# Kernel optimization log

Hardware: AMD Instinct MI355X
Metric: run time of the kernel (lower is better)

## Reference

```python
import jax, jax.numpy as jnp
import numpy as np

B, S_Q, S_KV = 4, 2048, 2048
D_MODEL, HEADS, D_QK, D_V = 1024, 16, 64, 64


def setup_inputs() -> dict:
    key = jax.random.key(0)
    ks = jax.random.split(key, 12)
    s = lambda fan_in: 1.0 / np.sqrt(fan_in)
    return {
        "x": jax.random.normal(ks[0], (B, S_Q, D_MODEL), jnp.float32),
        "encoder_output": jax.random.normal(ks[1], (B, S_KV, D_MODEL), jnp.float32),
        # per-head Linear weights stacked over heads: [H, D_MODEL, d_head]
        "Wq": jax.random.uniform(ks[2], (HEADS, D_MODEL, D_QK), jnp.float32, -s(D_MODEL), s(D_MODEL)),
        "bq": jax.random.uniform(ks[3], (HEADS, D_QK), jnp.float32, -s(D_MODEL), s(D_MODEL)),
        "Wk": jax.random.uniform(ks[4], (HEADS, D_MODEL, D_QK), jnp.float32, -s(D_MODEL), s(D_MODEL)),
        "bk": jax.random.uniform(ks[5], (HEADS, D_QK), jnp.float32, -s(D_MODEL), s(D_MODEL)),
        "Wv": jax.random.uniform(ks[6], (HEADS, D_MODEL, D_V), jnp.float32, -s(D_MODEL), s(D_MODEL)),
        "bv": jax.random.uniform(ks[7], (HEADS, D_V), jnp.float32, -s(D_MODEL), s(D_MODEL)),
        # output Linear: [H*D_V, D_MODEL]
        "Wo": jax.random.uniform(ks[8], (HEADS * D_V, D_MODEL), jnp.float32, -s(HEADS * D_V), s(HEADS * D_V)),
        "bo": jax.random.uniform(ks[9], (D_MODEL,), jnp.float32, -s(HEADS * D_V), s(HEADS * D_V)),
    }


def reference(x, encoder_output, Wq, bq, Wk, bk, Wv, bv, Wo, bo):
    # Batched equivalent of the per-head Python loop: project all heads at once.
    q = jnp.einsum("bqd,hde->bhqe", x, Wq) + bq[None, :, None, :]              # [B,H,Sq,dk]
    k = jnp.einsum("bsd,hde->bhse", encoder_output, Wk) + bk[None, :, None, :]  # [B,H,Skv,dk]
    v = jnp.einsum("bsd,hde->bhse", encoder_output, Wv) + bv[None, :, None, :]  # [B,H,Skv,dv]
    scale = 1.0 / jnp.sqrt(jnp.asarray(D_QK, x.dtype))
    scores = jnp.einsum("bhqe,bhse->bhqs", q, k) * scale                        # [B,H,Sq,Skv]
    attn = jax.nn.softmax(scores, axis=-1)
    heads = jnp.einsum("bhqs,bhse->bhqe", attn, v)                              # [B,H,Sq,dv]
    # concat heads on last dim (head order matches the torch list concat)
    multihead = heads.transpose(0, 2, 1, 3).reshape(x.shape[0], x.shape[1], HEADS * D_V)
    return multihead @ Wo + bo
```

## Files before the change

### kernel.cpp

```cpp
#include <hip/hip_runtime.h>
#include <hip/hip_bf16.h>
#include <stdint.h>

typedef unsigned short u16;
typedef __bf16 bf16x8 __attribute__((ext_vector_type(8)));
typedef float f32x4 __attribute__((ext_vector_type(4)));
typedef float f32x16 __attribute__((ext_vector_type(16)));
typedef unsigned short us8 __attribute__((ext_vector_type(8)));

__device__ __forceinline__ u16 f2bf(float f) {
  union { float f; uint32_t u; } v; v.f = f;
  uint32_t u = v.u;
  return (u16)((u + 0x7FFFu + ((u >> 16) & 1u)) >> 16);
}

__device__ __forceinline__ uint32_t cvtpk(float a, float b) {
  uint32_t r;
  asm("v_cvt_pk_bf16_f32 %0, %1, %2" : "=v"(r) : "v"(a), "v"(b));
  return r;
}

__device__ __forceinline__ void gload_lds16(const void* g, void* l) {
  __builtin_amdgcn_global_load_lds(
      (const __attribute__((address_space(1))) void*)(uintptr_t)g,
      (__attribute__((address_space(3))) void*)(uint32_t)(uintptr_t)l,
      16, 0, 0);
}

__device__ __forceinline__ float vsum16(f32x16 v) {
  float a = (v[0] + v[1]) + (v[2] + v[3]);
  float b = (v[4] + v[5]) + (v[6] + v[7]);
  float c = (v[8] + v[9]) + (v[10] + v[11]);
  float d = (v[12] + v[13]) + (v[14] + v[15]);
  return (a + b) + (c + d);
}

#define CROW(r, g) (((r) & 3) + 8 * ((r) >> 2) + 4 * (g))

__global__ __launch_bounds__(256) void cvt_all_k(
    const float* __restrict__ x, const float* __restrict__ enc,
    const float* __restrict__ Wq, const float* __restrict__ Wk,
    const float* __restrict__ Wv, const float* __restrict__ Wo,
    u16* __restrict__ xb, u16* __restrict__ eb,
    u16* __restrict__ wqb, u16* __restrict__ wkb,
    u16* __restrict__ wvb, u16* __restrict__ wob) {
  __shared__ float t[64][65];
  const int blk = blockIdx.x;
  const int tid = threadIdx.x;

  if (blk < 8192) {
    const float* in = (blk < 4096) ? x : enc;
    u16* out = (blk < 4096) ? xb : eb;
    size_t i = (size_t)(blk & 4095) * 256 + tid;
    const float4* p = (const float4*)in + i * 2;
    float4 a = p[0], b = p[1];
    us8 o;
    o[0] = f2bf(a.x); o[1] = f2bf(a.y); o[2] = f2bf(a.z); o[3] = f2bf(a.w);
    o[4] = f2bf(b.x); o[5] = f2bf(b.y); o[6] = f2bf(b.z); o[7] = f2bf(b.w);
    *(us8*)(out + i * 8) = o;
    return;
  }

  if (blk < 8960) {
    int r = blk - 8192;
    int z = r >> 8;
    const float* W = (z == 0) ? Wq : (z == 1) ? Wk : Wv;
    u16* o = (z == 0) ? wqb : (z == 1) ? wkb : wvb;
    const int h = (r & 255) >> 4, d0 = (r & 15) * 64;
    const float* Wb = W + ((size_t)h << 16) + (size_t)d0 * 64;
#pragma unroll
    for (int i = 0; i < 4; ++i) {
      int idx = tid + i * 256;
      int dl = idx >> 4, e4 = (idx & 15) << 2;
      float4 v = *(const float4*)(Wb + dl * 64 + e4);
      t[dl][e4 + 0] = v.x; t[dl][e4 + 1] = v.y; t[dl][e4 + 2] = v.z; t[dl][e4 + 3] = v.w;
    }
    __syncthreads();
#pragma unroll
    for (int i = 0; i < 2; ++i) {
      int idx = tid + i * 256;
      int e = idx >> 3, dc = (idx & 7) * 8;
      us8 w;
#pragma unroll
      for (int j = 0; j < 8; ++j) w[j] = f2bf(t[dc + j][e]);
      *(us8*)(o + ((size_t)(h * 64 + e)) * 1024 + d0 + dc) = w;
    }
    return;
  }

  {
    int r = blk - 8960;
    const int k0 = (r & 15) * 64, n0 = (r >> 4) * 64;
    const float* Wb = Wo + (size_t)k0 * 1024 + n0;
#pragma unroll
    for (int i = 0; i < 4; ++i) {
      int idx = tid + i * 256;
      int kl = idx >> 4, n4 = (idx & 15) << 2;
      float4 v = *(const float4*)(Wb + (size_t)kl * 1024 + n4);
      t[kl][n4 + 0] = v.x; t[kl][n4 + 1] = v.y; t[kl][n4 + 2] = v.z; t[kl][n4 + 3] = v.w;
    }
    __syncthreads();
#pragma unroll
    for (int i = 0; i < 2; ++i) {
      int idx = tid + i * 256;
      int n = idx >> 3, kc = (idx & 7) * 8;
      us8 w;
#pragma unroll
      for (int j = 0; j < 8; ++j) w[j] = f2bf(t[kc + j][n]);
      *(us8*)(wob + ((size_t)(n0 + n)) * 1024 + k0 + kc) = w;
    }
  }
}

__device__ __forceinline__ void gemm_core(const char* Ac, const char* Bc, int K,
                                          int m0, int n0, int tid,
                                          char* As0, char* As1, char* Bs0, char* Bs1,
                                          f32x4 (&acc)[4][4]) {
  const int wave = tid >> 6, lane = tid & 63;
  const int lo = lane & 15, hi = lane >> 4;
  const int wr = wave >> 1, wc = wave & 1;
  const int o0 = wave * 1024 + lane * 16;
  const int r0 = o0 >> 6, cb0 = o0 & 63;
  const int o1 = o0 + 4096;
  const int r1 = o1 >> 6, cb1 = o1 & 63;
  const size_t ksz = (size_t)K * 2;

  auto STAGE = [&](int t) {
    const size_t kb = (size_t)t * 64;
    char* Ad = (t & 1) ? As1 : As0;
    char* Bd = (t & 1) ? Bs1 : Bs0;
    gload_lds16(Ac + (size_t)(m0 + r0) * ksz + kb + cb0, Ad + o0);
    gload_lds16(Ac + (size_t)(m0 + r1) * ksz + kb + cb1, Ad + o1);
    gload_lds16(Bc + (size_t)(n0 + r0) * ksz + kb + cb0, Bd + o0);
    gload_lds16(Bc + (size_t)(n0 + r1) * ksz + kb + cb1, Bd + o1);
  };

  const int NK = K >> 5;
  STAGE(0);
  STAGE(1);

  for (int kk = 0; kk < NK; ++kk) {
    if (kk < NK - 1) {
      asm volatile("s_waitcnt vmcnt(4)" ::: "memory");
    } else {
      asm volatile("s_waitcnt vmcnt(0)" ::: "memory");
    }
    __builtin_amdgcn_s_barrier();
    __builtin_amdgcn_sched_barrier(0);
    const u16* Asb = (const u16*)((kk & 1) ? As1 : As0);
    const u16* Bsb = (const u16*)((kk & 1) ? Bs1 : Bs0);
    bf16x8 af[4], bfr[4];
#pragma unroll
    for (int i = 0; i < 4; ++i) {
      af[i]  = *(const bf16x8*)(Asb + (wr * 64 + i * 16 + lo) * 32 + hi * 8);
      bfr[i] = *(const bf16x8*)(Bsb + (wc * 64 + i * 16 + lo) * 32 + hi * 8);
    }
    asm volatile("s_waitcnt lgkmcnt(0)" ::: "memory");
    __builtin_amdgcn_sched_barrier(0);
    __builtin_amdgcn_s_barrier();
    if (kk + 2 < NK) STAGE(kk + 2);
    __builtin_amdgcn_s_setprio(1);
#pragma unroll
    for (int am = 0; am < 4; ++am)
#pragma unroll
      for (int bn = 0; bn < 4; ++bn)
        acc[am][bn] = __builtin_amdgcn_mfma_f32_16x16x32_bf16(af[am], bfr[bn], acc[am][bn], 0, 0, 0);
    __builtin_amdgcn_s_setprio(0);
  }
}

__global__ __launch_bounds__(256) void qkv_proj_k(
    const u16* __restrict__ xb, const u16* __restrict__ eb,
    const u16* __restrict__ wqb, const u16* __restrict__ wkvb,
    const float* __restrict__ bq, const float* __restrict__ bk_,
    const float* __restrict__ bv_,
    u16* __restrict__ Qg, u16* __restrict__ Kg, u16* __restrict__ Vt, float scale) {
  __shared__ __attribute__((aligned(16))) char As[2][8192];
  __shared__ __attribute__((aligned(16))) char Bs[2][8192];
  const int blk = blockIdx.x;
  const int tid = threadIdx.x;
  const int wave = tid >> 6, lane = tid & 63;
  const int lo = lane & 15, hi = lane >> 4;
  const int wr = wave >> 1, wc = wave & 1;

  f32x4 acc[4][4] = {};

  if (blk < 512) {
    const int n0 = (blk & 7) * 128, m0 = (blk >> 3) * 128;
    gemm_core((const char*)xb, (const char*)wqb, 1024, m0, n0, tid,
              As[0], As[1], Bs[0], Bs[1], acc);
#pragma unroll
    for (int bn = 0; bn < 4; ++bn) {
      int col = n0 + wc * 64 + bn * 16 + lo;
      float bb = bq[col];
      int hh = col >> 6, e = col & 63;
#pragma unroll
      for (int am = 0; am < 4; ++am) {
#pragma unroll
        for (int r = 0; r < 4; ++r) {
          int row = m0 + wr * 64 + am * 16 + hi * 4 + r;
          int b = row >> 11, s = row & 2047;
          Qg[(((size_t)(b * 16 + hh) * 2048 + s) << 6) + e] = f2bf((acc[am][bn][r] + bb) * scale);
        }
      }
    }
  } else {
    const int r_ = blk - 512;
    const int n0 = (r_ & 15) * 128, m0 = (r_ >> 4) * 128;
    gemm_core((const char*)eb, (const char*)wkvb, 1024, m0, n0, tid,
              As[0], As[1], Bs[0], Bs[1], acc);
    const bool isV = (n0 + wc * 64) >= 1024;
    if (!isV) {
#pragma unroll
      for (int bn = 0; bn < 4; ++bn) {
        int col = n0 + wc * 64 + bn * 16 + lo;
        float bb = bk_[col];
        int hh = col >> 6, e = col & 63;
#pragma unroll
        for (int am = 0; am < 4; ++am) {
#pragma unroll
          for (int r = 0; r < 4; ++r) {
            int row = m0 + wr * 64 + am * 16 + hi * 4 + r;
            int b = row >> 11, s = row & 2047;
            s = (s & ~12) | ((s & 4) << 1) | ((s & 8) >> 1);
            Kg[(((size_t)(b * 16 + hh) * 2048 + s) << 6) + e] = f2bf(acc[am][bn][r] + bb);
          }
        }
      }
    } else {
#pragma unroll
      for (int bn = 0; bn < 4; ++bn) {
        int c = (n0 + wc * 64 + bn * 16 + lo) - 1024;
        float bb = bv_[c];
        int hh = c >> 6, e = c & 63;
#pragma unroll
        for (int am = 0; am < 4; ++am) {
          int row = m0 + wr * 64 + am * 16 + hi * 4;
          int b = row >> 11, s = row & 2047;
          uint2 wv;
          wv.x = cvtpk(acc[am][bn][0] + bb, acc[am][bn][1] + bb);
          wv.y = cvtpk(acc[am][bn][2] + bb, acc[am][bn][3] + bb);
          *(uint2*)(Vt + (((size_t)(b * 16 + hh) * 64 + e) * 2048 + s)) = wv;
        }
      }
    }
  }
}

__global__ __launch_bounds__(256) void out_proj_k(const u16* __restrict__ A,
                                                  const u16* __restrict__ B,
                                                  const float* __restrict__ bias,
                                                  float* __restrict__ C, int M, int N, int K) {
  __shared__ __attribute__((aligned(16))) char As[2][8192];
  __shared__ __attribute__((aligned(16))) char Bs[2][8192];
  const int tid = threadIdx.x;
  const int wave = tid >> 6, lane = tid & 63;
  const int lo = lane & 15, hi = lane >> 4;
  const int wr = wave >> 1, wc = wave & 1;
  const int n0 = blockIdx.x * 128, m0 = blockIdx.y * 128;

  f32x4 acc[4][4] = {};
  gemm_core((const char*)A, (const char*)B, K, m0, n0, tid,
            As[0], As[1], Bs[0], Bs[1], acc);

#pragma unroll
  for (int bn = 0; bn < 4; ++bn) {
    int col = n0 + wc * 64 + bn * 16 + lo;
    float bb = bias[col];
#pragma unroll
    for (int am = 0; am < 4; ++am) {
#pragma unroll
      for (int r = 0; r < 4; ++r) {
        int row = m0 + wr * 64 + am * 16 + hi * 4 + r;
        C[(size_t)row * N + col] = acc[am][bn][r] + bb;
      }
    }
  }
}

__global__ __launch_bounds__(256, 4) void attn_k(const u16* __restrict__ Qg,
                                                 const u16* __restrict__ Kg,
                                                 const u16* __restrict__ Vtg,
                                                 u16* __restrict__ Hd) {
  const int W = blockIdx.x;
  const int bid = (W >> 7) * 128 + (W & 7) * 16 + ((W >> 3) & 15);
  const int bh = bid >> 4;
  const int q0 = (bid & 15) * 128;
  const int tid = threadIdx.x;
  const int w = tid >> 6, lane = tid & 63;
  const int q31 = lane & 31, g = lane >> 5;

  __shared__ __attribute__((aligned(16))) char LB[2][16384];

  bf16x8 qf0, qf1, qf2, qf3;
  {
    const char* Qrow = (const char*)(Qg + ((size_t)bh * 2048 + q0 + w * 32 + q31) * 64) + g * 16;
    qf0 = *(const bf16x8*)(Qrow);
    qf1 = *(const bf16x8*)(Qrow + 32);
    qf2 = *(const bf16x8*)(Qrow + 64);
    qf3 = *(const bf16x8*)(Qrow + 96);
  }

  f32x16 acc0 = {}, acc1 = {};
  float lrun = 0.f;

  const int lrow = lane >> 3;
  const int scol = ((lane & 7) ^ lrow) << 4;
  const char* kp = (const char*)Kg + (size_t)bh * 262144 + (size_t)(w * 16 + lrow) * 128 + scol;
  const char* vp = (const char*)Vtg + (size_t)bh * 262144 + (size_t)(w * 16 + lrow) * 4096 + scol;

  auto STAGE = [&](int c) {
    char* kb = &LB[c][0] + w * 2048;
    char* vb = kb + 8192;
    gload_lds16(kp, kb);
    gload_lds16(kp + 1024, kb + 1024);
    gload_lds16(vp, vb);
    gload_lds16(vp + 32768, vb + 1024);
    kp += 8192;
    vp += 128;
  };

  STAGE(0);

  const int swz = (q31 & 7) << 4;
  const int krow = q31 * 128;
  const int ko0 = (g * 16) ^ swz;
  const int ko1 = (32 + g * 16) ^ swz;
  const int ko2 = (64 + g * 16) ^ swz;
  const int ko3 = (96 + g * 16) ^ swz;

  int cur = 0;
  for (int t = 0; t < 32; ++t) {
    asm volatile("s_waitcnt vmcnt(0)" ::: "memory");
    __builtin_amdgcn_s_barrier();
    asm volatile("" ::: "memory");
    if (t < 31) STAGE(cur ^ 1);

    const char* Kc = &LB[cur][0];
    const char* Vc = Kc + 8192;

    f32x16 p0 = {}, p1 = {};
    __builtin_amdgcn_s_setprio(1);
    {
      bf16x8 kf;
      kf = *(const bf16x8*)(Kc + krow + ko0);
      p0 = __builtin_amdgcn_mfma_f32_32x32x16_bf16(kf, qf0, p0, 0, 0, 0);
      kf = *(const bf16x8*)(Kc + 4096 + krow + ko0);
      p1 = __builtin_amdgcn_mfma_f32_32x32x16_bf16(kf, qf0, p1, 0, 0, 0);
      kf = *(const bf16x8*)(Kc + krow + ko1);
      p0 = __builtin_amdgcn_mfma_f32_32x32x16_bf16(kf, qf1, p0, 0, 0, 0);
      kf = *(const bf16x8*)(Kc + 4096 + krow + ko1);
      p1 = __builtin_amdgcn_mfma_f32_32x32x16_bf16(kf, qf1, p1, 0, 0, 0);
      kf = *(const bf16x8*)(Kc + krow + ko2);
      p0 = __builtin_amdgcn_mfma_f32_32x32x16_bf16(kf, qf2, p0, 0, 0, 0);
      kf = *(const bf16x8*)(Kc + 4096 + krow + ko2);
      p1 = __builtin_amdgcn_mfma_f32_32x32x16_bf16(kf, qf2, p1, 0, 0, 0);
      kf = *(const bf16x8*)(Kc + krow + ko3);
      p0 = __builtin_amdgcn_mfma_f32_32x32x16_bf16(kf, qf3, p0, 0, 0, 0);
      kf = *(const bf16x8*)(Kc + 4096 + krow + ko3);
      p1 = __builtin_amdgcn_mfma_f32_32x32x16_bf16(kf, qf3, p1, 0, 0, 0);
    }
    __builtin_amdgcn_s_setprio(0);

#pragma unroll
    for (int i = 0; i < 16; ++i) p0[i] = __builtin_amdgcn_exp2f(p0[i]);
#pragma unroll
    for (int i = 0; i < 16; ++i) p1[i] = __builtin_amdgcn_exp2f(p1[i]);

    float rs = vsum16(p0) + vsum16(p1);
    {
      float ra = rs, rb = rs;
      asm("v_permlane32_swap_b32 %0, %1" : "+v"(ra), "+v"(rb));
      rs += g ? ra : rb;
    }
    lrun += rs;

    union PU { uint32_t u[4]; bf16x8 v; } a0, a1, a2, a3;
    a0.u[0] = cvtpk(p0[0], p0[1]);   a0.u[1] = cvtpk(p0[2], p0[3]);
    a0.u[2] = cvtpk(p0[4], p0[5]);   a0.u[3] = cvtpk(p0[6], p0[7]);
    a1.u[0] = cvtpk(p0[8], p0[9]);   a1.u[1] = cvtpk(p0[10], p0[11]);
    a1.u[2] = cvtpk(p0[12], p0[13]); a1.u[3] = cvtpk(p0[14], p0[15]);
    a2.u[0] = cvtpk(p1[0], p1[1]);   a2.u[1] = cvtpk(p1[2], p1[3]);
    a2.u[2] = cvtpk(p1[4], p1[5]);   a2.u[3] = cvtpk(p1[6], p1[7]);
    a3.u[0] = cvtpk(p1[8], p1[9]);   a3.u[1] = cvtpk(p1[10], p1[11]);
    a3.u[2] = cvtpk(p1[12], p1[13]); a3.u[3] = cvtpk(p1[14], p1[15]);

    __builtin_amdgcn_s_setprio(1);
    {
      bf16x8 vf;
      vf = *(const bf16x8*)(Vc + krow + ko0);
      acc0 = __builtin_amdgcn_mfma_f32_32x32x16_bf16(a0.v, vf, acc0, 0, 0, 0);
      vf = *(const bf16x8*)(Vc + 4096 + krow + ko0);
      acc1 = __builtin_amdgcn_mfma_f32_32x32x16_bf16(a0.v, vf, acc1, 0, 0, 0);
      vf = *(const bf16x8*)(Vc + krow + ko1);
      acc0 = __builtin_amdgcn_mfma_f32_32x32x16_bf16(a1.v, vf, acc0, 0, 0, 0);
      vf = *(const bf16x8*)(Vc + 4096 + krow + ko1);
      acc1 = __builtin_amdgcn_mfma_f32_32x32x16_bf16(a1.v, vf, acc1, 0, 0, 0);
      vf = *(const bf16x8*)(Vc + krow + ko2);
      acc0 = __builtin_amdgcn_mfma_f32_32x32x16_bf16(a2.v, vf, acc0, 0, 0, 0);
      vf = *(const bf16x8*)(Vc + 4096 + krow + ko2);
      acc1 = __builtin_amdgcn_mfma_f32_32x32x16_bf16(a2.v, vf, acc1, 0, 0, 0);
      vf = *(const bf16x8*)(Vc + krow + ko3);
      acc0 = __builtin_amdgcn_mfma_f32_32x32x16_bf16(a3.v, vf, acc0, 0, 0, 0);
      vf = *(const bf16x8*)(Vc + 4096 + krow + ko3);
      acc1 = __builtin_amdgcn_mfma_f32_32x32x16_bf16(a3.v, vf, acc1, 0, 0, 0);
    }
    __builtin_amdgcn_s_setprio(0);

    cur ^= 1;
  }

  float linv = 1.f / lrun;
  const int b = bh >> 4, h = bh & 15;
  u16* Ho = Hd + ((size_t)b * 2048 + q0 + w * 32) * 1024 + h * 64;
#pragma unroll
  for (int r = 0; r < 16; ++r) {
    float iv = __shfl(linv, CROW(r, g));
    int q = CROW(r, g);
    u16* row = Ho + (size_t)q * 1024;
    row[q31]      = f2bf(acc0[r] * iv);
    row[32 + q31] = f2bf(acc1[r] * iv);
  }
}


extern "C" void kernel_launch(void* const* d_in, const int* in_sizes, int n_in,
                              void* d_out, int out_size, void* d_ws, size_t ws_size,
                              hipStream_t stream) {
  const float* x   = (const float*)d_in[0];
  const float* enc = (const float*)d_in[1];
  const float* Wq  = (const float*)d_in[2];
  const float* bq  = (const float*)d_in[3];
  const float* Wk  = (const float*)d_in[4];
  const float* bk  = (const float*)d_in[5];
  const float* Wv  = (const float*)d_in[6];
  const float* bv  = (const float*)d_in[7];
  const float* Wo  = (const float*)d_in[8];
  const float* bo  = (const float*)d_in[9];
  float* out = (float*)d_out;
  char* ws = (char*)d_ws;

  const size_t SZ = 16u * 1024u * 1024u;
  u16* xb  = (u16*)(ws + 0 * SZ);
  u16* eb  = (u16*)(ws + 1 * SZ);
  u16* Qg  = (u16*)(ws + 2 * SZ);
  u16* Kg  = (u16*)(ws + 3 * SZ);
  u16* vtb = (u16*)(ws + 4 * SZ);
  u16* wqb = (u16*)(ws + 5 * SZ + 0u * (2u << 20));
  u16* wkb = (u16*)(ws + 5 * SZ + 1u * (2u << 20));
  u16* wob = (u16*)(ws + 5 * SZ + 3u * (2u << 20));
  u16* hd  = xb;

  const float cs = 0.18033688011112042f;

  cvt_all_k<<<9216, 256, 0, stream>>>(x, enc, Wq, Wk, Wv, Wo, xb, eb, wqb, wkb,
                                      (u16*)(ws + 5 * SZ + 2u * (2u << 20)), wob);

  qkv_proj_k<<<1536, 256, 0, stream>>>(xb, eb, wqb, wkb, bq, bk, bv, Qg, Kg, vtb, cs);

  attn_k<<<1024, 256, 0, stream>>>(Qg, Kg, vtb, hd);

  out_proj_k<<<dim3(8, 64), 256, 0, stream>>>(hd, wob, bo, out, 8192, 1024, 1024);
}
```

Baseline: 196.0 us.

## Fuse fp32 activation bf16 conversion into QKV projection GEMM loads

Removes the separate pass that converted x and encoder_output to bf16. The QKV GEMM now streams fp32 activation tiles straight into swizzled LDS and converts them to bf16 in registers before the MFMAs. This saves writing and re-reading the bf16 activation copies. In exchange the A tiles need twice the LDS and global load bytes per stage, and the same fp32 data is re-read by several column blocks.

```diff
diff --git a/kernel.cpp b/kernel.cpp
--- a/kernel.cpp
+++ b/kernel.cpp
@@ -37,36 +37,21 @@
 
 #define CROW(r, g) (((r) & 3) + 8 * ((r) >> 2) + 4 * (g))
 
-__global__ __launch_bounds__(256) void cvt_all_k(
-    const float* __restrict__ x, const float* __restrict__ enc,
+__global__ __launch_bounds__(256) void cvt_w_k(
     const float* __restrict__ Wq, const float* __restrict__ Wk,
     const float* __restrict__ Wv, const float* __restrict__ Wo,
-    u16* __restrict__ xb, u16* __restrict__ eb,
     u16* __restrict__ wqb, u16* __restrict__ wkb,
     u16* __restrict__ wvb, u16* __restrict__ wob) {
   __shared__ float t[64][65];
   const int blk = blockIdx.x;
   const int tid = threadIdx.x;
 
-  if (blk < 8192) {
-    const float* in = (blk < 4096) ? x : enc;
-    u16* out = (blk < 4096) ? xb : eb;
-    size_t i = (size_t)(blk & 4095) * 256 + tid;
-    const float4* p = (const float4*)in + i * 2;
-    float4 a = p[0], b = p[1];
-    us8 o;
-    o[0] = f2bf(a.x); o[1] = f2bf(a.y); o[2] = f2bf(a.z); o[3] = f2bf(a.w);
-    o[4] = f2bf(b.x); o[5] = f2bf(b.y); o[6] = f2bf(b.z); o[7] = f2bf(b.w);
-    *(us8*)(out + i * 8) = o;
-    return;
-  }
-
-  if (blk < 8960) {
-    int r = blk - 8192;
-    int z = r >> 8;
+  if (blk < 768) {
+    int z = blk >> 8;
     const float* W = (z == 0) ? Wq : (z == 1) ? Wk : Wv;
     u16* o = (z == 0) ? wqb : (z == 1) ? wkb : wvb;
-    const int h = (r & 255) >> 4, d0 = (r & 15) * 64;
+    const int r = blk & 255;
+    const int h = r >> 4, d0 = (r & 15) * 64;
     const float* Wb = W + ((size_t)h << 16) + (size_t)d0 * 64;
 #pragma unroll
     for (int i = 0; i < 4; ++i) {
@@ -89,7 +74,7 @@
   }
 
   {
-    int r = blk - 8960;
+    int r = blk - 768;
     const int k0 = (r & 15) * 64, n0 = (r >> 4) * 64;
     const float* Wb = Wo + (size_t)k0 * 1024 + n0;
 #pragma unroll
@@ -169,13 +154,88 @@
   }
 }
 
+__device__ __forceinline__ void gemm_core_f32a(const float* Af, const char* Bc, int K,
+                                               int m0, int n0, int tid,
+                                               char* Afs0, char* Afs1, char* Bs0, char* Bs1,
+                                               f32x4 (&acc)[4][4]) {
+  const int wave = tid >> 6, lane = tid & 63;
+  const int lo = lane & 15, hi = lane >> 4;
+  const int wr = wave >> 1, wc = wave & 1;
+  const int ao = wave * 1024 + lane * 16;
+  const int arow_base = (ao >> 7);
+  const int ascol = (ao & 127) ^ ((lane >> 3) << 4);
+  const int o0 = wave * 1024 + lane * 16;
+  const int r0 = o0 >> 6, cb0 = o0 & 63;
+  const int o1 = o0 + 4096;
+  const int r1 = o1 >> 6, cb1 = o1 & 63;
+  const size_t kszB = (size_t)K * 2;
+  const size_t kszA = (size_t)K * 4;
+
+  auto STAGE = [&](int t) {
+    char* Ad = (t & 1) ? Afs1 : Afs0;
+    char* Bd = (t & 1) ? Bs1 : Bs0;
+    const size_t kbA = (size_t)t * 128;
+    const size_t kbB = (size_t)t * 64;
+#pragma unroll
+    for (int j = 0; j < 4; ++j) {
+      gload_lds16((const char*)Af + (size_t)(m0 + arow_base + j * 32) * kszA + kbA + ascol,
+                  Ad + j * 4096 + ao);
+    }
+    gload_lds16(Bc + (size_t)(n0 + r0) * kszB + kbB + cb0, Bd + o0);
+    gload_lds16(Bc + (size_t)(n0 + r1) * kszB + kbB + cb1, Bd + o1);
+  };
+
+  const int NK = K >> 5;
+  STAGE(0);
+  STAGE(1);
+
+  const int aswz = (lo & 7) << 4;
+
+  for (int kk = 0; kk < NK; ++kk) {
+    if (kk < NK - 1) {
+      asm volatile("s_waitcnt vmcnt(6)" ::: "memory");
+    } else {
+      asm volatile("s_waitcnt vmcnt(0)" ::: "memory");
+    }
+    __builtin_amdgcn_s_barrier();
+    __builtin_amdgcn_sched_barrier(0);
+    const char* Asb = (kk & 1) ? Afs1 : Afs0;
+    const u16* Bsb = (const u16*)((kk & 1) ? Bs1 : Bs0);
+    bf16x8 af[4], bfr[4];
+#pragma unroll
+    for (int i = 0; i < 4; ++i) {
+      const int row = wr * 64 + i * 16 + lo;
+      f32x4 a0 = *(const f32x4*)(Asb + row * 128 + ((hi * 32) ^ aswz));
+      f32x4 a1 = *(const f32x4*)(Asb + row * 128 + ((hi * 32 + 16) ^ aswz));
+      union { uint32_t u[4]; bf16x8 v; } cv;
+      cv.u[0] = cvtpk(a0[0], a0[1]);
+      cv.u[1] = cvtpk(a0[2], a0[3]);
+      cv.u[2] = cvtpk(a1[0], a1[1]);
+      cv.u[3] = cvtpk(a1[2], a1[3]);
+      af[i] = cv.v;
+      bfr[i] = *(const bf16x8*)(Bsb + (wc * 64 + i * 16 + lo) * 32 + hi * 8);
+    }
+    asm volatile("s_waitcnt lgkmcnt(0)" ::: "memory");
+    __builtin_amdgcn_sched_barrier(0);
+    __builtin_amdgcn_s_barrier();
+    if (kk + 2 < NK) STAGE(kk + 2);
+    __builtin_amdgcn_s_setprio(1);
+#pragma unroll
+    for (int am = 0; am < 4; ++am)
+#pragma unroll
+      for (int bn = 0; bn < 4; ++bn)
+        acc[am][bn] = __builtin_amdgcn_mfma_f32_16x16x32_bf16(af[am], bfr[bn], acc[am][bn], 0, 0, 0);
+    __builtin_amdgcn_s_setprio(0);
+  }
+}
+
 __global__ __launch_bounds__(256) void qkv_proj_k(
-    const u16* __restrict__ xb, const u16* __restrict__ eb,
+    const float* __restrict__ x, const float* __restrict__ enc,
     const u16* __restrict__ wqb, const u16* __restrict__ wkvb,
     const float* __restrict__ bq, const float* __restrict__ bk_,
     const float* __restrict__ bv_,
     u16* __restrict__ Qg, u16* __restrict__ Kg, u16* __restrict__ Vt, float scale) {
-  __shared__ __attribute__((aligned(16))) char As[2][8192];
+  __shared__ __attribute__((aligned(16))) char As[2][16384];
   __shared__ __attribute__((aligned(16))) char Bs[2][8192];
   const int blk = blockIdx.x;
   const int tid = threadIdx.x;
@@ -187,8 +247,8 @@
 
   if (blk < 512) {
     const int n0 = (blk & 7) * 128, m0 = (blk >> 3) * 128;
-    gemm_core((const char*)xb, (const char*)wqb, 1024, m0, n0, tid,
-              As[0], As[1], Bs[0], Bs[1], acc);
+    gemm_core_f32a(x, (const char*)wqb, 1024, m0, n0, tid,
+                   As[0], As[1], Bs[0], Bs[1], acc);
 #pragma unroll
     for (int bn = 0; bn < 4; ++bn) {
       int col = n0 + wc * 64 + bn * 16 + lo;
@@ -207,8 +267,8 @@
   } else {
     const int r_ = blk - 512;
     const int n0 = (r_ & 15) * 128, m0 = (r_ >> 4) * 128;
-    gemm_core((const char*)eb, (const char*)wkvb, 1024, m0, n0, tid,
-              As[0], As[1], Bs[0], Bs[1], acc);
+    gemm_core_f32a(enc, (const char*)wkvb, 1024, m0, n0, tid,
+                   As[0], As[1], Bs[0], Bs[1], acc);
     const bool isV = (n0 + wc * 64) >= 1024;
     if (!isV) {
 #pragma unroll
@@ -441,22 +501,20 @@
   char* ws = (char*)d_ws;
 
   const size_t SZ = 16u * 1024u * 1024u;
-  u16* xb  = (u16*)(ws + 0 * SZ);
-  u16* eb  = (u16*)(ws + 1 * SZ);
+  u16* hd  = (u16*)(ws + 0 * SZ);
   u16* Qg  = (u16*)(ws + 2 * SZ);
   u16* Kg  = (u16*)(ws + 3 * SZ);
   u16* vtb = (u16*)(ws + 4 * SZ);
   u16* wqb = (u16*)(ws + 5 * SZ + 0u * (2u << 20));
   u16* wkb = (u16*)(ws + 5 * SZ + 1u * (2u << 20));
+  u16* wvb = (u16*)(ws + 5 * SZ + 2u * (2u << 20));
   u16* wob = (u16*)(ws + 5 * SZ + 3u * (2u << 20));
-  u16* hd  = xb;
 
   const float cs = 0.18033688011112042f;
 
-  cvt_all_k<<<9216, 256, 0, stream>>>(x, enc, Wq, Wk, Wv, Wo, xb, eb, wqb, wkb,
-                                      (u16*)(ws + 5 * SZ + 2u * (2u << 20)), wob);
-
-  qkv_proj_k<<<1536, 256, 0, stream>>>(xb, eb, wqb, wkb, bq, bk, bv, Qg, Kg, vtb, cs);
+  cvt_w_k<<<1024, 256, 0, stream>>>(Wq, Wk, Wv, Wo, wqb, wkb, wvb, wob);
+
+  qkv_proj_k<<<1536, 256, 0, stream>>>(x, enc, wqb, wkb, bq, bk, bv, Qg, Kg, vtb, cs);
 
   attn_k<<<1024, 256, 0, stream>>>(Qg, Kg, vtb, hd);
 
```

Result: slower. 209.6 us (+6.9%).
